# Performance work log

Measured on AMD Instinct MI355X. Metric: run time of the kernel, lower is better.

Reference implementation:

```python
import jax, jax.numpy as jnp
import numpy as np

N, E, D, H, DH, M = 100000, 1600000, 128, 8, 16, 3  # nodes, edges, model_dim, heads, head_dim, views
NEG = -1e9


def setup_inputs() -> dict:
    key = jax.random.key(0)
    ks = jax.random.split(key, 12)
    x = jax.random.normal(ks[0], (N, D), jnp.float32)
    src = jax.random.randint(ks[1], (E,), 0, N)
    dst = jax.random.randint(ks[2], (E,), 0, N)
    pi = jax.random.uniform(ks[3], (N, H, M), jnp.float32)
    pi = pi / pi.sum(-1, keepdims=True)  # router mixture over views
    view_w = jax.random.uniform(ks[4], (E, M), jnp.float32)
    s = 1.0 / np.sqrt(D)
    Wq = jax.random.normal(ks[5], (D, D), jnp.float32) * s
    Wk = jax.random.normal(ks[6], (D, D), jnp.float32) * s
    Wv = jax.random.normal(ks[7], (D, D), jnp.float32) * s
    bq = jax.random.normal(ks[8], (D,), jnp.float32) * 0.02
    bk = jax.random.normal(ks[9], (D,), jnp.float32) * 0.02
    bv = jax.random.normal(ks[10], (D,), jnp.float32) * 0.02
    return {"x": x, "pi": pi, "view_w": view_w, "Wq": Wq, "bq": bq,
            "Wk": Wk, "bk": bk, "Wv": Wv, "bv": bv, "src": src, "dst": dst}


def reference(x, pi, view_w, Wq, bq, Wk, bk, Wv, bv, src, dst):
    n = x.shape[0]
    q = (x @ Wq + bq).reshape(n, H, DH)
    k = (x @ Wk + bk).reshape(n, H, DH)
    v = (x @ Wv + bv).reshape(n, H, DH)
    # per-edge mixture weight: sum over views of pi[dst] * view_w  -> [E, H]
    mix = jnp.einsum('ehm,em->eh', pi[dst], view_w)
    raw = jnp.einsum('ehd,ehd->eh', q[dst], k[src]) / jnp.sqrt(jnp.float32(DH))
    scores = raw + jnp.log(jnp.clip(mix, 1e-8))  # adjacency_mode == 'bias'
    valid = mix > 0
    masked = jnp.where(valid, scores, NEG)
    # scatter-softmax over incoming edges per (node, head)
    smax = jax.ops.segment_max(masked, dst, num_segments=n)
    expv = jnp.where(valid, jnp.exp(masked - smax[dst]), 0.0)
    ssum = jax.ops.segment_sum(expv, dst, num_segments=n)
    attn = expv / jnp.maximum(ssum[dst], 1e-8)  # [E, H]
    # weighted scatter-sum aggregation -> [N, H, DH]
    node_states = jax.ops.segment_sum(v[src] * attn[:, :, None], dst, num_segments=n)
    return node_states, attn
```

## Files before the change

### kernel.cpp

```cpp
#include <hip/hip_runtime.h>
#include <hip/hip_bf16.h>
#include <math.h>

#define NEG -1e9f
#define SCAN_CHUNK 2048

typedef _Float16 half8 __attribute__((ext_vector_type(8)));
typedef _Float16 half16v __attribute__((ext_vector_type(16)));
typedef float floatx4 __attribute__((ext_vector_type(4)));


__global__ void hist_kernel(const int* __restrict__ dst, int* __restrict__ counts, int e) {
    int i = blockIdx.x * blockDim.x + threadIdx.x;
    if (i < e) atomicAdd(&counts[dst[i]], 1);
}

__global__ __launch_bounds__(256) void scan_block_sums(const int* __restrict__ counts,
                                                       int* __restrict__ bsum, int n) {
    __shared__ int sd[256];
    int t = threadIdx.x;
    int base = blockIdx.x * SCAN_CHUNK + t * 8;
    int s = 0;
#pragma unroll
    for (int j = 0; j < 8; ++j) {
        int idx = base + j;
        if (idx < n) s += counts[idx];
    }
    sd[t] = s;
    __syncthreads();
    for (int off = 128; off > 0; off >>= 1) {
        if (t < off) sd[t] += sd[t + off];
        __syncthreads();
    }
    if (t == 0) bsum[blockIdx.x] = sd[0];
}

__global__ void scan_wave(int* bsum, int nb) {
    int lane = threadIdx.x;
    int orig = (lane < nb) ? bsum[lane] : 0;
    int v = orig;
    for (int off = 1; off < 64; off <<= 1) {
        int t = __shfl_up(v, off, 64);
        if (lane >= off) v += t;
    }
    if (lane < nb) bsum[lane] = v - orig;
}

__global__ __launch_bounds__(256) void scan_write(const int* __restrict__ counts,
                                                  const int* __restrict__ bsum,
                                                  int* __restrict__ row_ptr,
                                                  int* __restrict__ cursor,
                                                  int n, int total) {
    __shared__ int sd[256];
    int t = threadIdx.x;
    int base = blockIdx.x * SCAN_CHUNK + t * 8;
    int v[8];
    int s = 0;
#pragma unroll
    for (int j = 0; j < 8; ++j) {
        int idx = base + j;
        v[j] = (idx < n) ? counts[idx] : 0;
        s += v[j];
    }
    sd[t] = s;
    __syncthreads();
    for (int off = 1; off < 256; off <<= 1) {
        int tmp = 0;
        if (t >= off) tmp = sd[t - off];
        __syncthreads();
        if (t >= off) sd[t] += tmp;
        __syncthreads();
    }
    int run = bsum[blockIdx.x] + sd[t] - s;
#pragma unroll
    for (int j = 0; j < 8; ++j) {
        int idx = base + j;
        if (idx < n) {
            row_ptr[idx] = run;
            cursor[idx] = run;
            run += v[j];
        }
    }
    if (blockIdx.x == 0 && t == 0) row_ptr[n] = total;
}

__global__ void fill_csr(const int* __restrict__ dst, int* cursor,
                         int* __restrict__ csr, int e) {
    int i = blockIdx.x * blockDim.x + threadIdx.x;
    if (i < e) {
        int p = atomicAdd(&cursor[dst[i]], 1);
        csr[p] = i;
    }
}


__global__ __launch_bounds__(256) void convert_x(const float* __restrict__ x,
                                                 _Float16* __restrict__ xh, int total8) {
    int i = blockIdx.x * blockDim.x + threadIdx.x;
    if (i < total8) {
        const float4* s = (const float4*)x + i * 2;
        float4 a = s[0], b = s[1];
        half8 h;
        h[0] = (_Float16)a.x; h[1] = (_Float16)a.y; h[2] = (_Float16)a.z; h[3] = (_Float16)a.w;
        h[4] = (_Float16)b.x; h[5] = (_Float16)b.y; h[6] = (_Float16)b.z; h[7] = (_Float16)b.w;
        *((half8*)xh + i) = h;
    }
}

__global__ __launch_bounds__(256) void prep_w(const float* __restrict__ Wq,
                                              const float* __restrict__ Wk,
                                              const float* __restrict__ Wv,
                                              _Float16* __restrict__ wt) {
    const float* W = (blockIdx.x == 0) ? Wq : (blockIdx.x == 1) ? Wk : Wv;
    _Float16* out = wt + (size_t)blockIdx.x * 16384;
    int t = threadIdx.x;
    for (int r = 0; r < 64; ++r) {
        int idx = r * 256 + t;
        int k = idx >> 7, nn = idx & 127;
        out[nn * 128 + k] = (_Float16)W[idx];
    }
}


#define LDP 136

__global__ __launch_bounds__(256) void qkv_mfma(
    const _Float16* __restrict__ xh, const _Float16* __restrict__ wt,
    const float* __restrict__ bq, const float* __restrict__ bk,
    const float* __restrict__ bv,
    _Float16* __restrict__ qh, _Float16* __restrict__ kh, _Float16* __restrict__ vh,
    int n) {
    __shared__ __align__(16) _Float16 xs[128 * LDP];
    __shared__ __align__(16) _Float16 ws[128 * LDP];

    int t = threadIdx.x;
    int tile0 = blockIdx.x * 128;
    int sel = blockIdx.y;
    const _Float16* wsel = wt + (size_t)sel * 16384;
    const float* bias = (sel == 0) ? bq : (sel == 1) ? bk : bv;
    _Float16* out = (sel == 0) ? qh : (sel == 1) ? kh : vh;

#pragma unroll
    for (int r = 0; r < 8; ++r) {
        int id = r * 256 + t;
        int row = id >> 4, c8 = id & 15;
        int grow = tile0 + row;
        half8 val = (half8)(_Float16)0;
        if (grow < n) val = *((const half8*)(xh + (size_t)grow * 128) + c8);
        *((half8*)(xs + row * LDP) + c8) = val;
        half8 wv = *((const half8*)(wsel + row * 128) + c8);
        *((half8*)(ws + row * LDP) + c8) = wv;
    }
    __syncthreads();

    int wave = t >> 6, lane = t & 63;
    int wm = (wave & 1) * 64, wn = (wave >> 1) * 64;
    int lrow = lane & 15, quad = lane >> 4;

    floatx4 acc[4][4];
#pragma unroll
    for (int i = 0; i < 4; ++i)
#pragma unroll
        for (int j = 0; j < 4; ++j) acc[i][j] = (floatx4)0.f;

#pragma unroll
    for (int kk = 0; kk < 4; ++kk) {
        int kbase = kk * 32 + quad * 8;
        half8 a[4], b[4];
#pragma unroll
        for (int i = 0; i < 4; ++i)
            a[i] = *(const half8*)(xs + (wm + i * 16 + lrow) * LDP + kbase);
#pragma unroll
        for (int j = 0; j < 4; ++j)
            b[j] = *(const half8*)(ws + (wn + j * 16 + lrow) * LDP + kbase);
#pragma unroll
        for (int i = 0; i < 4; ++i)
#pragma unroll
            for (int j = 0; j < 4; ++j)
                acc[i][j] = __builtin_amdgcn_mfma_f32_16x16x32_f16(a[i], b[j], acc[i][j], 0, 0, 0);
    }

#pragma unroll
    for (int i = 0; i < 4; ++i) {
#pragma unroll
        for (int j = 0; j < 4; ++j) {
            int col = wn + j * 16 + lrow;
            float bv_ = bias[col];
#pragma unroll
            for (int r = 0; r < 4; ++r) {
                int row = wm + i * 16 + quad * 4 + r;
                int grow = tile0 + row;
                if (grow < n) out[(size_t)grow * 128 + col] = (_Float16)(acc[i][j][r] + bv_);
            }
        }
    }
}


__global__ __launch_bounds__(256) void edge_attn(
    const _Float16* __restrict__ qh, const _Float16* __restrict__ kh,
    const _Float16* __restrict__ vh, const float* __restrict__ pi,
    const float* __restrict__ view_w, const int* __restrict__ src,
    const int* __restrict__ row_ptr, const int* __restrict__ csr,
    float* __restrict__ node_out, float* attn_out, int n) {
    int t = threadIdx.x;
    int node = blockIdx.x * 32 + (t >> 3);
    int h = t & 7;
    if (node >= n) return;

    half16v qv = *(const half16v*)(qh + (size_t)node * 128 + h * 16);
    float qf[16];
#pragma unroll
    for (int j = 0; j < 16; ++j) qf[j] = (float)qv[j];

    float p0 = pi[node * 24 + h * 3 + 0];
    float p1 = pi[node * 24 + h * 3 + 1];
    float p2 = pi[node * 24 + h * 3 + 2];
    int beg = row_ptr[node], end = row_ptr[node + 1];

    float m = -INFINITY, l = 0.f;
    float acc[16];
#pragma unroll
    for (int j = 0; j < 16; ++j) acc[j] = 0.f;

    for (int i = beg; i < end; ++i) {
        int e = csr[i];
        int s0 = src[e];
        float w0 = view_w[e * 3 + 0], w1 = view_w[e * 3 + 1], w2 = view_w[e * 3 + 2];
        float mix = fmaf(p0, w0, fmaf(p1, w1, p2 * w2));
        half16v kv = *(const half16v*)(kh + (size_t)s0 * 128 + h * 16);
        float dot = 0.f;
#pragma unroll
        for (int j = 0; j < 16; ++j) dot = fmaf(qf[j], (float)kv[j], dot);
        float s = (mix > 0.f) ? (dot * 0.25f + __logf(fmaxf(mix, 1e-8f))) : NEG;
        attn_out[(size_t)e * 8 + h] = s;
        if (s > 0.5f * NEG) {
            if (s > m) {
                float sc = __expf(m - s);
                l *= sc;
#pragma unroll
                for (int j = 0; j < 16; ++j) acc[j] *= sc;
                m = s;
            }
            float w = __expf(s - m);
            l += w;
            half16v vv = *(const half16v*)(vh + (size_t)s0 * 128 + h * 16);
#pragma unroll
            for (int j = 0; j < 16; ++j) acc[j] = fmaf(w, (float)vv[j], acc[j]);
        }
    }

    float inv = 1.f / fmaxf(l, 1e-8f);
    float4* op = (float4*)(node_out + (size_t)node * 128 + h * 16);
#pragma unroll
    for (int j = 0; j < 4; ++j)
        op[j] = make_float4(acc[4 * j] * inv, acc[4 * j + 1] * inv,
                            acc[4 * j + 2] * inv, acc[4 * j + 3] * inv);

    for (int i = beg; i < end; ++i) {
        int e = csr[i];
        float s = attn_out[(size_t)e * 8 + h];
        float w = (s <= 0.5f * NEG) ? 0.f : __expf(s - m);
        attn_out[(size_t)e * 8 + h] = w * inv;
    }
}


extern "C" void kernel_launch(void* const* d_in, const int* in_sizes, int n_in,
                              void* d_out, int out_size, void* d_ws, size_t ws_size,
                              hipStream_t stream) {
    const float* x  = (const float*)d_in[0];
    const float* pi = (const float*)d_in[1];
    const float* vw = (const float*)d_in[2];
    const float* Wq = (const float*)d_in[3];
    const float* bq = (const float*)d_in[4];
    const float* Wk = (const float*)d_in[5];
    const float* bk = (const float*)d_in[6];
    const float* Wv = (const float*)d_in[7];
    const float* bv = (const float*)d_in[8];
    const int* src  = (const int*)d_in[9];
    const int* dst  = (const int*)d_in[10];

    int n = in_sizes[0] / 128;
    int e = in_sizes[9];

    _Float16* xh = (_Float16*)d_ws;
    _Float16* qh = xh + (size_t)n * 128;
    _Float16* kh = qh + (size_t)n * 128;
    _Float16* vh = kh + (size_t)n * 128;
    _Float16* wt = vh + (size_t)n * 128;
    int* counts  = (int*)(wt + 3 * 16384);
    int* cursor  = counts + n;
    int* row_ptr = cursor + n;
    int* csr     = row_ptr + n + 1;
    int* bsum    = csr + e;

    float* node_out = (float*)d_out;
    float* attn_out = node_out + (size_t)n * 128;

    hipMemsetAsync(counts, 0, (size_t)n * sizeof(int), stream);

    int eb = (e + 255) / 256;
    hist_kernel<<<eb, 256, 0, stream>>>(dst, counts, e);

    int nb = (n + SCAN_CHUNK - 1) / SCAN_CHUNK;
    scan_block_sums<<<nb, 256, 0, stream>>>(counts, bsum, n);
    scan_wave<<<1, 64, 0, stream>>>(bsum, nb);
    scan_write<<<nb, 256, 0, stream>>>(counts, bsum, row_ptr, cursor, n, e);
    fill_csr<<<eb, 256, 0, stream>>>(dst, cursor, csr, e);

    int tot8 = (n * 128) / 8;
    convert_x<<<(tot8 + 255) / 256, 256, 0, stream>>>(x, xh, tot8);
    prep_w<<<3, 256, 0, stream>>>(Wq, Wk, Wv, wt);

    int gtiles = (n + 127) / 128;
    qkv_mfma<<<dim3(gtiles, 3), 256, 0, stream>>>(xh, wt, bq, bk, bv, qh, kh, vh, n);

    int gb = (n + 31) / 32;
    edge_attn<<<gb, 256, 0, stream>>>(qh, kh, vh, pi, vw, src, row_ptr, csr,
                                      node_out, attn_out, n);
}
```

Baseline: 738.3 us.

## Drop online softmax max tracking; write unnormalized fp16 weights and normalize in edge pass

The per-(node,head) loop stops doing online-max rescaling. It computes p = mix*exp(dot/4) directly, with no log and no running max, and always loads V, prefetching the next edge's index and view weights one step ahead. Unnormalized weights are stored as fp16 in a workspace buffer along with per-node inverse sums. A new coalesced per-edge kernel then writes the normalized fp32 attention. This replaces the scattered read-modify-write second pass over CSR edges with a streaming pass, and removes the branchy rescaling. The trade-off is possible overflow without max subtraction and fp16 precision loss in the attention output.

```diff
diff --git a/kernel.cpp b/kernel.cpp
--- a/kernel.cpp
+++ b/kernel.cpp
@@ -2,7 +2,6 @@
 #include <hip/hip_bf16.h>
 #include <math.h>
 
-#define NEG -1e9f
 #define SCAN_CHUNK 2048
 
 typedef _Float16 half8 __attribute__((ext_vector_type(8)));
@@ -202,7 +201,8 @@
     const _Float16* __restrict__ vh, const float* __restrict__ pi,
     const float* __restrict__ view_w, const int* __restrict__ src,
     const int* __restrict__ row_ptr, const int* __restrict__ csr,
-    float* __restrict__ node_out, float* attn_out, int n) {
+    float* __restrict__ node_out, float* __restrict__ invb,
+    _Float16* __restrict__ pbuf, int n) {
     int t = threadIdx.x;
     int node = blockIdx.x * 32 + (t >> 3);
     int h = t & 7;
@@ -218,50 +218,71 @@
     float p2 = pi[node * 24 + h * 3 + 2];
     int beg = row_ptr[node], end = row_ptr[node + 1];
 
-    float m = -INFINITY, l = 0.f;
+    float l = 0.f;
     float acc[16];
 #pragma unroll
     for (int j = 0; j < 16; ++j) acc[j] = 0.f;
 
+    int e_n = 0, s_n = 0;
+    float wa_n = 0.f, wb_n = 0.f, wc_n = 0.f;
+    if (beg < end) {
+        e_n = csr[beg]; s_n = src[e_n];
+        const float* vp_ = view_w + (size_t)e_n * 3;
+        wa_n = vp_[0]; wb_n = vp_[1]; wc_n = vp_[2];
+    }
+
     for (int i = beg; i < end; ++i) {
-        int e = csr[i];
-        int s0 = src[e];
-        float w0 = view_w[e * 3 + 0], w1 = view_w[e * 3 + 1], w2 = view_w[e * 3 + 2];
-        float mix = fmaf(p0, w0, fmaf(p1, w1, p2 * w2));
-        half16v kv = *(const half16v*)(kh + (size_t)s0 * 128 + h * 16);
-        float dot = 0.f;
-#pragma unroll
-        for (int j = 0; j < 16; ++j) dot = fmaf(qf[j], (float)kv[j], dot);
-        float s = (mix > 0.f) ? (dot * 0.25f + __logf(fmaxf(mix, 1e-8f))) : NEG;
-        attn_out[(size_t)e * 8 + h] = s;
-        if (s > 0.5f * NEG) {
-            if (s > m) {
-                float sc = __expf(m - s);
-                l *= sc;
-#pragma unroll
-                for (int j = 0; j < 16; ++j) acc[j] *= sc;
-                m = s;
-            }
-            float w = __expf(s - m);
-            l += w;
-            half16v vv = *(const half16v*)(vh + (size_t)s0 * 128 + h * 16);
-#pragma unroll
-            for (int j = 0; j < 16; ++j) acc[j] = fmaf(w, (float)vv[j], acc[j]);
+        int e = e_n, s0 = s_n;
+        float wa = wa_n, wb = wb_n, wc = wc_n;
+
+        const half16v* kp = (const half16v*)(kh + (size_t)s0 * 128 + h * 16);
+        half16v kv = kp[0];
+        const half16v* vp = (const half16v*)(vh + (size_t)s0 * 128 + h * 16);
+        half16v vv = vp[0];
+
+        if (i + 1 < end) {
+            e_n = csr[i + 1]; s_n = src[e_n];
+            const float* vpn = view_w + (size_t)e_n * 3;
+            wa_n = vpn[0]; wb_n = vpn[1]; wc_n = vpn[2];
         }
+
+        float mix = fmaf(p0, wa, fmaf(p1, wb, p2 * wc));
+        float d = 0.f;
+#pragma unroll
+        for (int j = 0; j < 16; ++j) d = fmaf(qf[j], (float)kv[j], d);
+
+        float p = (mix > 0.f) ? mix * __expf(d * 0.25f) : 0.f;
+        pbuf[(size_t)e * 8 + h] = (_Float16)p;
+        l += p;
+#pragma unroll
+        for (int j = 0; j < 16; ++j) acc[j] = fmaf(p, (float)vv[j], acc[j]);
     }
 
     float inv = 1.f / fmaxf(l, 1e-8f);
+    invb[(size_t)node * 8 + h] = inv;
+
     float4* op = (float4*)(node_out + (size_t)node * 128 + h * 16);
 #pragma unroll
     for (int j = 0; j < 4; ++j)
         op[j] = make_float4(acc[4 * j] * inv, acc[4 * j + 1] * inv,
                             acc[4 * j + 2] * inv, acc[4 * j + 3] * inv);
-
-    for (int i = beg; i < end; ++i) {
-        int e = csr[i];
-        float s = attn_out[(size_t)e * 8 + h];
-        float w = (s <= 0.5f * NEG) ? 0.f : __expf(s - m);
-        attn_out[(size_t)e * 8 + h] = w * inv;
+}
+
+
+__global__ __launch_bounds__(256) void attn_norm(
+    const _Float16* __restrict__ pbuf, const int* __restrict__ dst,
+    const float* __restrict__ invb, float* __restrict__ attn_out, int e) {
+    int i = blockIdx.x * blockDim.x + threadIdx.x;
+    if (i < e) {
+        int d = dst[i];
+        half8 p = *((const half8*)pbuf + i);
+        const float4* iv = (const float4*)(invb + (size_t)d * 8);
+        float4 i0 = iv[0], i1 = iv[1];
+        float4* op = (float4*)(attn_out + (size_t)i * 8);
+        op[0] = make_float4((float)p[0] * i0.x, (float)p[1] * i0.y,
+                            (float)p[2] * i0.z, (float)p[3] * i0.w);
+        op[1] = make_float4((float)p[4] * i1.x, (float)p[5] * i1.y,
+                            (float)p[6] * i1.z, (float)p[7] * i1.w);
     }
 }
 
@@ -289,7 +310,9 @@
     _Float16* kh = qh + (size_t)n * 128;
     _Float16* vh = kh + (size_t)n * 128;
     _Float16* wt = vh + (size_t)n * 128;
-    int* counts  = (int*)(wt + 3 * 16384);
+    _Float16* pbuf = wt + 3 * 16384;
+    float* invb  = (float*)(pbuf + (size_t)e * 8);
+    int* counts  = (int*)(invb + (size_t)n * 8);
     int* cursor  = counts + n;
     int* row_ptr = cursor + n;
     int* csr     = row_ptr + n + 1;
@@ -318,5 +341,6 @@
 
     int gb = (n + 31) / 32;
     edge_attn<<<gb, 256, 0, stream>>>(qh, kh, vh, pi, vw, src, row_ptr, csr,
-                                      node_out, attn_out, n);
-}
+                                      node_out, invb, pbuf, n);
+    attn_norm<<<eb, 256, 0, stream>>>(pbuf, dst, invb, attn_out, e);
+}
```

Measured after the change: 667.9 us. 1.11x faster.
